# Kernel tuning notes

Measured on AMD Instinct MI355X. Metric: run time of the kernel, lower is better.

## Reference

```python
import jax, jax.numpy as jnp
import numpy as np

NUM_PATCHES = 10
SIGMA = 4.0            # size_exp_deadzone
PAD_X = 16             # padding_deadzone_size_x
PAD_Y = 16             # padding_deadzone_size_y
DEADZONE_EXP = True
HARD_CUTOUT = True     # deadzone_hard_cutout == 1
HARD_CUTOUT_SIZE = 4.0


def setup_inputs() -> dict:
    key = jax.random.key(0)
    k1, k2, k3, k4 = jax.random.split(key, 4)
    B, C, H, W = 8, 1, 256, 256
    D, KH, KW = 64, 1, 33
    inp = {
        "input": jax.random.normal(k1, (B, C, H, W), dtype=jnp.float32),
        "dictionary_filter": jax.random.normal(k2, (64, C, 33, 33), dtype=jnp.float32),
        "dictionary": jax.random.normal(k3, (64, C, 33, 33), dtype=jnp.float32),
        "dictionary_prior": jax.random.uniform(k4, (64,), dtype=jnp.float32),
    }
    return inp


def _fourier_convolution(contour, dictionary_filter):
    # contour: [B,C,H,W], dictionary_filter: [D,C,kh,kw] (kh,kw odd)
    B, C, H, W = contour.shape
    D, _, kh, kw = dictionary_filter.shape
    filt = jnp.flip(dictionary_filter, axis=(-2, -1))
    padded = jnp.zeros((D, C, H, W), dtype=contour.dtype).at[:, :, :kh, :kw].set(filt)
    padded = jnp.roll(padded, shift=(-(kh // 2), -(kw // 2)), axis=(-2, -1))
    filt_fft = jnp.fft.rfft2(padded)                 # [D,C,H,W//2+1]
    contour_fft = jnp.fft.rfft2(contour)             # [B,C,H,W//2+1]
    # [B,D,C,H,W] -> sum over channel C -> [B,D,H,W]
    conv = jnp.fft.irfft2(contour_fft[:, None] * filt_fft[None], s=(H, W)).sum(axis=2)
    return conv


def reference(input, dictionary_filter, dictionary, dictionary_prior):
    B, C, H, W = input.shape
    dt = input.dtype
    conv = _fourier_convolution(input, dictionary_filter)  # [B,D,H,W]

    use_map = jnp.ones((B, H, W), dtype=dt)
    if PAD_X > 0:
        use_map = use_map.at[:, :PAD_X, :].set(0.0).at[:, -PAD_X:, :].set(0.0)
    if PAD_Y > 0:
        use_map = use_map.at[:, :, :PAD_Y].set(0.0).at[:, :, -PAD_Y:].set(0.0)

    xs = jnp.arange(H, dtype=dt)
    ys = jnp.arange(W, dtype=dt)
    batch_idx = jnp.arange(B)

    def step(use_map, _):
        # search tensor: conv * use_map * prior  -> [B,D,H,W]
        search = conv * use_map[:, None] * dictionary_prior[None, :, None, None]
        flat = search.reshape(B, -1)
        idx = jnp.argmax(flat, axis=1)                    # [B]
        ov0 = jnp.max(flat, axis=1)                       # saliency incl. prior
        d = idx // (H * W)
        rem = idx % (H * W)
        px = rem // W
        py = rem % W
        ov1 = conv[batch_idx, d, px, py]                  # raw overlap
        # deadzone centered at (px,py)
        dx = xs[None, :] - px[:, None].astype(dt)         # [B,H]
        dy = ys[None, :] - py[:, None].astype(dt)         # [B,W]
        dist2 = dx[:, :, None] ** 2 + dy[:, None, :] ** 2  # [B,H,W]
        if DEADZONE_EXP:
            tmap = 1.0 - jnp.exp(-dist2 / (2.0 * SIGMA ** 2))
        else:
            tmap = jnp.ones_like(dist2)
        if HARD_CUTOUT:
            tmap = tmap * jnp.where(dist2 <= HARD_CUTOUT_SIZE ** 2, 0.0, 1.0)
        new_use = use_map * tmap
        new_use = new_use / jnp.max(new_use, axis=(1, 2), keepdims=True)
        pos = jnp.stack([d, px, py], axis=1)              # [B,3]
        ov = jnp.stack([ov0, ov1], axis=1)                # [B,2]
        return new_use, (pos, ov)

    _, (pos, ov) = jax.lax.scan(step, use_map, None, length=NUM_PATCHES)
    position_found = jnp.transpose(pos, (1, 0, 2))  # [B, num_patches, 3] int
    overlap_found = jnp.transpose(ov, (1, 0, 2))    # [B, num_patches, 2]
    return position_found, overlap_found
```

## Files before the change

kernel.cpp:

```cpp
#include <hip/hip_runtime.h>

typedef unsigned long long u64;
typedef unsigned int u32;
typedef unsigned short ushort_t;

using f32x16 = __attribute__((ext_vector_type(16))) float;
using f32x4  = __attribute__((ext_vector_type(4))) float;
using short8 = __attribute__((ext_vector_type(8))) short;

#define NB 8
#define NPIX 65536
#define CAND_CAP 65536
#define MARGIN 45.0f

__device__ __forceinline__ u32 fsort(float f){
  u32 u = __float_as_uint(f);
  return (u & 0x80000000u) ? ~u : (u | 0x80000000u);
}
__device__ __forceinline__ float funsort(u32 s){
  u32 u = (s & 0x80000000u) ? (s ^ 0x80000000u) : ~s;
  return __uint_as_float(u);
}
__device__ __forceinline__ u32 rneb(float f){
  u32 x = __float_as_uint(f);
  return (x + 0x7fffu + ((x >> 16) & 1u)) >> 16;
}
__device__ __forceinline__ float bf2f(u32 h){ return __uint_as_float(h << 16); }

__global__ __launch_bounds__(256) void prep_kernel(
    const float* __restrict__ filt, const float* __restrict__ prior,
    ushort_t* __restrict__ afh, ushort_t* __restrict__ acolh,
    float* __restrict__ fcorner, float* __restrict__ priorR,
    float* __restrict__ filtT4, float* __restrict__ filtC,
    u32* __restrict__ ncand, u32* __restrict__ mmax)
{
  int t = blockIdx.x * 256 + threadIdx.x;
  if (t == 0) *ncand = 0u;
  if (t < 8) mmax[t] = 0u;
  for (int i = t; i < 67584; i += 16384){
    int j = i & 7; int fidx = i >> 3; int lane = fidx & 63; int rest = fidx >> 6;
    int dt = rest & 1; int kc = (rest >> 1) & 1; int fy = rest >> 2;
    int d = dt * 32 + (lane & 31);
    int fx = 16 * kc + 8 * (lane >> 5) + j;
    afh[i] = (ushort_t)rneb(filt[d * 1089 + fy * 33 + fx]);
  }
  for (int i = t; i < 2048; i += 16384){
    int j = i & 7; int fidx = i >> 3; int lane = fidx & 63; int rest = fidx >> 6;
    int dt = rest & 1; int kc = rest >> 1;
    int d = dt * 32 + (lane & 31);
    int fy = 16 * kc + 8 * (lane >> 5) + j;
    acolh[i] = (ushort_t)rneb(filt[d * 1089 + fy * 33 + 32]);
  }
  for (int i = t; i < 2048; i += 16384){
    int reg = i & 15; int rest = i >> 4; int lane = rest & 63; int dt = rest >> 6;
    int d = dt * 32 + (reg & 3) + 8 * (reg >> 2) + 4 * (lane >> 5);
    fcorner[i] = filt[d * 1089 + 1088];
    priorR[i] = prior[d];
  }
  for (int i = t; i < 67584; i += 16384){
    int e = i & 3; int d = (i >> 2) & 63; int q = (i >> 8) & 7; int fy = i >> 11;
    filtT4[i] = filt[d * 1089 + fy * 33 + 4 * q + e];
  }
  for (int i = t; i < 2112; i += 16384){
    int d = i & 63; int fy = i >> 6;
    filtC[i] = filt[d * 1089 + fy * 33 + 32];
  }
}

__device__ __forceinline__ u32 funnel(u32 hi, u32 lo, int sh){
  return (u32)((((u64)hi << 32) | (u64)lo) >> sh);
}
template<int J>
__device__ __forceinline__ short8 extractf(uint4 P0, uint4 P1, int sh){
  u32 W[8] = {P0.x, P0.y, P0.z, P0.w, P1.x, P1.y, P1.z, P1.w};
  uint4 t;
  t.x = funnel(W[J + 1], W[J + 0], sh);
  t.y = funnel(W[J + 2], W[J + 1], sh);
  t.z = funnel(W[J + 3], W[J + 2], sh);
  t.w = funnel(W[J + 4], W[J + 3], sh);
  return __builtin_bit_cast(short8, t);
}
__device__ __forceinline__ f32x16 zero16(){
  f32x16 v;
  #pragma unroll
  for (int i = 0; i < 16; ++i) v[i] = 0.f;
  return v;
}

template<int J>
__device__ __forceinline__ void conv_body(
    const char* ldsc, const ushort_t* lds16, int w, int l, int tX,
    const short8* __restrict__ afh8, const short8* __restrict__ acol8,
    const f32x4* __restrict__ fcp, const f32x4* __restrict__ prp,
    u64* __restrict__ pb, int sh)
{
  const int c = l & 31, h = l >> 5;
  const int y0 = w;
  int cob0[2], cob1[2];
  #pragma unroll
  for (int kc = 0; kc < 2; ++kc){
    int yp = (y0 + 8 * c + 16 * kc + 8 * h - 16) & 255;
    int b0 = yp >> 3, b1 = (b0 + 1) & 31;
    cob0[kc] = b0 * 16; cob1[kc] = b1 * 16;
  }
  const int cc = (y0 + 8 * c + 16) & 255;

#define LA(DST, FY)                                                           \
  { _Pragma("unroll")                                                         \
    for (int kc = 0; kc < 2; ++kc)                                            \
      _Pragma("unroll")                                                       \
      for (int dt = 0; dt < 2; ++dt)                                          \
        DST[kc][dt] = afh8[(((FY) * 2 + kc) * 2 + dt) * 64 + l]; }

#define LW(S, ROWI)                                                           \
  { const char* rb_ = ldsc + (ROWI) * 512;                                    \
    s##S##k0p0 = *(const uint4*)(rb_ + cob0[0]);                              \
    s##S##k0p1 = *(const uint4*)(rb_ + cob1[0]);                              \
    s##S##k1p0 = *(const uint4*)(rb_ + cob0[1]);                              \
    s##S##k1p1 = *(const uint4*)(rb_ + cob1[1]); }

#define CPH(SA, SB, ACUR, ANXT, FYP, DOPF)                                    \
  { if (DOPF){ LA(ANXT, FYP) }                                                \
    short8 b0k0 = extractf<J>(s##SA##k0p0, s##SA##k0p1, sh);                  \
    short8 b0k1 = extractf<J>(s##SA##k1p0, s##SA##k1p1, sh);                  \
    short8 b1k0 = extractf<J>(s##SB##k0p0, s##SB##k0p1, sh);                  \
    short8 b1k1 = extractf<J>(s##SB##k1p0, s##SB##k1p1, sh);                  \
    acc[0][0] = __builtin_amdgcn_mfma_f32_32x32x16_bf16(ACUR[0][0], b0k0, acc[0][0], 0, 0, 0); \
    acc[0][0] = __builtin_amdgcn_mfma_f32_32x32x16_bf16(ACUR[1][0], b0k1, acc[0][0], 0, 0, 0); \
    acc[0][1] = __builtin_amdgcn_mfma_f32_32x32x16_bf16(ACUR[0][1], b0k0, acc[0][1], 0, 0, 0); \
    acc[0][1] = __builtin_amdgcn_mfma_f32_32x32x16_bf16(ACUR[1][1], b0k1, acc[0][1], 0, 0, 0); \
    acc[1][0] = __builtin_amdgcn_mfma_f32_32x32x16_bf16(ACUR[0][0], b1k0, acc[1][0], 0, 0, 0); \
    acc[1][0] = __builtin_amdgcn_mfma_f32_32x32x16_bf16(ACUR[1][0], b1k1, acc[1][0], 0, 0, 0); \
    acc[1][1] = __builtin_amdgcn_mfma_f32_32x32x16_bf16(ACUR[0][1], b1k0, acc[1][1], 0, 0, 0); \
    acc[1][1] = __builtin_amdgcn_mfma_f32_32x32x16_bf16(ACUR[1][1], b1k1, acc[1][1], 0, 0, 0); }

  for (int g0 = 0; g0 < 2; ++g0){
    const int r0 = g0 * 2;
    f32x16 acc[2][2];
    #pragma unroll
    for (int nr = 0; nr < 2; ++nr)
      #pragma unroll
      for (int dt = 0; dt < 2; ++dt) acc[nr][dt] = zero16();

    uint4 s0k0p0, s0k0p1, s0k1p0, s0k1p1;
    uint4 s1k0p0, s1k0p1, s1k1p0, s1k1p1;
    short8 aA[2][2], aB[2][2];

    LW(0, r0)
    LW(1, r0 + 1)
    LA(aA, 0)

    #pragma unroll 1
    for (int fy2 = 0; fy2 < 32; fy2 += 2){
      CPH(0, 1, aA, aB, fy2 + 1, true)
      LW(0, r0 + fy2 + 2)
      CPH(1, 0, aB, aA, fy2 + 2, true)
      LW(1, r0 + fy2 + 3)
    }
    CPH(0, 1, aA, aB, 0, false)

    #pragma unroll
    for (int nr = 0; nr < 2; ++nr){
      #pragma unroll
      for (int kc = 0; kc < 2; ++kc){
        int base = (r0 + nr + 16 * kc + 8 * h) * 512 + cc * 2;
        u32 v0 = *(const ushort_t*)(ldsc + base + 0 * 512);
        u32 v1 = *(const ushort_t*)(ldsc + base + 1 * 512);
        u32 v2 = *(const ushort_t*)(ldsc + base + 2 * 512);
        u32 v3 = *(const ushort_t*)(ldsc + base + 3 * 512);
        u32 v4 = *(const ushort_t*)(ldsc + base + 4 * 512);
        u32 v5 = *(const ushort_t*)(ldsc + base + 5 * 512);
        u32 v6 = *(const ushort_t*)(ldsc + base + 6 * 512);
        u32 v7 = *(const ushort_t*)(ldsc + base + 7 * 512);
        uint4 t;
        t.x = v0 | (v1 << 16); t.y = v2 | (v3 << 16);
        t.z = v4 | (v5 << 16); t.w = v6 | (v7 << 16);
        short8 Bc = __builtin_bit_cast(short8, t);
        #pragma unroll
        for (int dt = 0; dt < 2; ++dt)
          acc[nr][dt] = __builtin_amdgcn_mfma_f32_32x32x16_bf16(
              acol8[(kc * 2 + dt) * 64 + l], Bc, acc[nr][dt], 0, 0, 0);
      }
    }

    #pragma unroll
    for (int nr = 0; nr < 2; ++nr){
      float cv = bf2f((u32)lds16[(r0 + nr + 32) * 256 + cc]);
      float bv = -3e38f; int bd = 0;
      #pragma unroll
      for (int dt = 0; dt < 2; ++dt){
        #pragma unroll
        for (int q = 0; q < 4; ++q){
          f32x4 fc4 = fcp[(dt * 64 + l) * 4 + q];
          f32x4 pr4 = prp[(dt * 64 + l) * 4 + q];
          #pragma unroll
          for (int e = 0; e < 4; ++e){
            int reg = q * 4 + e;
            float s = (acc[nr][dt][reg] + fc4[e] * cv) * pr4[e];
            int d = dt * 32 + e + 8 * q + 4 * h;
            if (s > bv || (s == bv && d < bd)){ bv = s; bd = d; }
          }
        }
      }
      int x = tX + r0 + nr;
      int y = y0 + 8 * c;
      u64 key = ((u64)fsort(bv) << 32) | (u64)(63 - bd);
      u64 other = __shfl_xor(key, 32);
      if (other > key) key = other;
      if (h == 0) pb[(x << 8) | y] = key;
    }
  }
#undef CPH
#undef LW
#undef LA
}

__global__ __launch_bounds__(512) void conv_mfma(
    const float* __restrict__ input,
    const ushort_t* __restrict__ afh, const ushort_t* __restrict__ acolh,
    const float* __restrict__ fcorner, const float* __restrict__ priorR,
    u64* __restrict__ packed)
{
  __shared__ ushort_t lds[9216];
  const int bS = blockIdx.x;
  const int b  = blockIdx.y;
  const int tX = bS * 4;
  const int tid = threadIdx.x;

  const float* inb = input + b * NPIX;
  for (int k = tid; k < 1152; k += 512){
    int r = k >> 5, u = k & 31;
    int gx = (tX - 16 + r) & 255;
    const float* src = inb + (gx << 8) + (u << 3);
    float4 v1 = *(const float4*)(src);
    float4 v2 = *(const float4*)(src + 4);
    uint4 t;
    t.x = rneb(v1.x) | (rneb(v1.y) << 16);
    t.y = rneb(v1.z) | (rneb(v1.w) << 16);
    t.z = rneb(v2.x) | (rneb(v2.y) << 16);
    t.w = rneb(v2.z) | (rneb(v2.w) << 16);
    *(uint4*)((char*)lds + r * 512 + u * 16) = t;
  }
  __syncthreads();

  const int w = tid >> 6, l = tid & 63;
  u64* pb = packed + b * NPIX;
  const int sh = 16 * (w & 1);
  const char* ldsc = (const char*)lds;
  const short8* afh8 = (const short8*)afh;
  const short8* acol8 = (const short8*)acolh;
  const f32x4* fcp = (const f32x4*)fcorner;
  const f32x4* prp = (const f32x4*)priorR;

  switch ((w >> 1) & 3){
    case 0: conv_body<0>(ldsc, lds, w, l, tX, afh8, acol8, fcp, prp, pb, sh); break;
    case 1: conv_body<1>(ldsc, lds, w, l, tX, afh8, acol8, fcp, prp, pb, sh); break;
    case 2: conv_body<2>(ldsc, lds, w, l, tX, afh8, acol8, fcp, prp, pb, sh); break;
    default: conv_body<3>(ldsc, lds, w, l, tX, afh8, acol8, fcp, prp, pb, sh); break;
  }
}

__global__ __launch_bounds__(256) void bmax_kernel(const u64* __restrict__ packed,
                                                   u32* __restrict__ mmax){
  const int b = blockIdx.y, blk = blockIdx.x, tid = threadIdx.x;
  const u32* ph = (const u32*)(packed + b * NPIX);
  u32 m = 0;
  for (int k = tid; k < 2048; k += 256) m = max(m, ph[2 * (blk * 2048 + k) + 1]);
  __shared__ u32 red[256];
  red[tid] = m; __syncthreads();
  for (int s = 128; s > 0; s >>= 1){
    if (tid < s) red[tid] = max(red[tid], red[tid + s]);
    __syncthreads();
  }
  if (tid == 0) atomicMax(&mmax[b], red[0]);
}

__global__ __launch_bounds__(256) void collect_kernel(const u64* __restrict__ packed,
    const u32* __restrict__ mmax, u32* __restrict__ ncand, u32* __restrict__ cand){
  const int b = blockIdx.y, blk = blockIdx.x, tid = threadIdx.x;
  float M = funsort(mmax[b]);
  u32 tu = fsort(M - MARGIN);
  const u32* ph = (const u32*)(packed + b * NPIX);
  for (int k = tid; k < 2048; k += 256){
    int p = blk * 2048 + k;
    u32 v = ph[2 * p + 1];
    if (v >= tu){
      u32 slot = atomicAdd(ncand, 1u);
      if (slot < CAND_CAP) cand[slot] = ((u32)b << 16) | (u32)p;
    }
  }
}

__global__ __launch_bounds__(256) void rerank_kernel(
    const float* __restrict__ input, const float* __restrict__ filtT4,
    const float* __restrict__ filtC, const float* __restrict__ prior,
    const u32* __restrict__ ncand, const u32* __restrict__ cand,
    u64* __restrict__ packed)
{
  const int lane = threadIdx.x & 63;
  const int wv = threadIdx.x >> 6;
  int n = (int)min(*ncand, (u32)CAND_CAP);
  float pv = prior[lane];
  for (int i = blockIdx.x * 4 + wv; i < n; i += 4096){
    u32 v = cand[i];
    int b = v >> 16, p = v & 0xffff;
    int px = p >> 8, py = p & 255;
    if (px < 16 || px >= 240 || py < 16 || py >= 240) continue;
    int yc = py - 16;
    float s0 = 0.f, s1 = 0.f, s2 = 0.f, s3 = 0.f;
    for (int fy = 0; fy < 33; ++fy){
      const float* ir = input + b * NPIX + ((px + fy - 16) << 8) + yc;
      const float* ft = filtT4 + fy * 2048 + lane * 4;
      #pragma unroll
      for (int q = 0; q < 8; ++q){
        const float4 fv = *(const float4*)(ft + q * 256);
        s0 = fmaf(fv.x, ir[4*q+0], s0);
        s1 = fmaf(fv.y, ir[4*q+1], s1);
        s2 = fmaf(fv.z, ir[4*q+2], s2);
        s3 = fmaf(fv.w, ir[4*q+3], s3);
      }
      s0 = fmaf(filtC[fy * 64 + lane], ir[32], s0);
    }
    float s = (s0 + s2) + (s1 + s3);
    u64 key = ((u64)fsort(s * pv) << 32) | (u64)(63 - lane);
    #pragma unroll
    for (int off = 32; off; off >>= 1){
      u64 o = __shfl_down(key, off);
      if (o > key) key = o;
    }
    if (lane == 0) packed[b * NPIX + p] = key;
  }
}

__global__ __launch_bounds__(1024) void greedy_kernel(
    const u64* __restrict__ packed, const float* __restrict__ prior,
    float* __restrict__ out)
{
  const int b = blockIdx.x;
  const int tid = threadIdx.x;
  const u64* pb = packed + b * NPIX;
  const u32* ph = (const u32*)pb;

  const int x = tid >> 2;
  const int ybase = (tid & 3) << 6;
  const int pbase = (x << 8) + ybase;

  float s[64];
  const bool rowin = (x >= 16 && x < 240);
  #pragma unroll
  for (int i = 0; i < 64; ++i){
    int y = ybase + i;
    float bvv = funsort(ph[2 * (pbase + i) + 1]);
    s[i] = (rowin && y >= 16 && y < 240) ? bvv : 0.0f;
  }
  float tm = -3e38f; int tp = pbase;
  #pragma unroll
  for (int i = 0; i < 64; ++i){
    if (s[i] > tm){ tm = s[i]; tp = pbase + i; }
  }

  __shared__ u64 warr[16];
  __shared__ int spx, spy;
  if (tid == 0){ spx = -100000; spy = -100000; }
  __syncthreads();

  for (int t = 0; t < 10; ++t){
    const int px = spx, py = spy;
    if (px >= 0){
      int dxr = x - px;
      if (dxr >= -24 && dxr <= 24){
        int lo = py - 24 - ybase;
        int hi = py + 24 - ybase;
        if (lo < 64 && hi >= 0){
          float dx2 = (float)(dxr * dxr);
          tm = -3e38f; tp = pbase;
          #pragma unroll
          for (int i = 0; i < 64; ++i){
            if (i >= lo && i <= hi){
              float dy = (float)(ybase + i - py);
              float d2 = dx2 + dy * dy;
              float tmap = 1.f - __expf(d2 * -0.03125f);
              if (d2 <= 16.f) tmap = 0.f;
              s[i] *= tmap;
            }
            if (s[i] > tm){ tm = s[i]; tp = pbase + i; }
          }
        }
      }
    }
    u64 key = ((u64)fsort(tm) << 32) | (u64)(0xFFFFu ^ (u32)tp);
    #pragma unroll
    for (int off = 32; off; off >>= 1){
      u64 o = __shfl_down(key, off);
      if (o > key) key = o;
    }
    if ((tid & 63) == 0) warr[tid >> 6] = key;
    __syncthreads();
    if (tid < 64){
      u64 k2 = (tid < 16) ? warr[tid] : 0ull;
      #pragma unroll
      for (int off = 8; off; off >>= 1){
        u64 o = __shfl_down(k2, off);
        if (o > k2) k2 = o;
      }
      if (tid == 0){
        int id = 0xFFFF ^ (int)(k2 & 0xFFFFull);
        float v = funsort((u32)(k2 >> 32));
        u64 pk = pb[id];
        int d = 63 - (int)(pk & 63ull);
        float bvv = funsort((u32)(pk >> 32));
        int xx = id >> 8, yy = id & 255;
        out[b * 30 + t * 3 + 0] = (float)d;
        out[b * 30 + t * 3 + 1] = (float)xx;
        out[b * 30 + t * 3 + 2] = (float)yy;
        out[240 + b * 20 + t * 2 + 0] = v;
        out[240 + b * 20 + t * 2 + 1] = bvv / prior[d];
        spx = xx; spy = yy;
      }
    }
    __syncthreads();
  }
}

extern "C" void kernel_launch(void* const* d_in, const int* in_sizes, int n_in,
                              void* d_out, int out_size, void* d_ws, size_t ws_size,
                              hipStream_t stream)
{
  const float* input = (const float*)d_in[0];
  const float* filt  = (const float*)d_in[1];
  const float* prior = (const float*)d_in[3];
  float* out = (float*)d_out;

  char* ws = (char*)d_ws;
  u64*      packed  = (u64*)(ws);
  u32*      ncand   = (u32*)  (ws + 4194304);
  u32*      mmax    = (u32*)  (ws + 4194368);
  ushort_t* afh     = (ushort_t*)(ws + 4194432);
  ushort_t* acolh   = (ushort_t*)(ws + 4329600);
  float*    fcorner = (float*)(ws + 4333696);
  float*    priorR  = (float*)(ws + 4341888);
  u32*      cand    = (u32*)  (ws + 4350080);
  float*    filtT4  = (float*)(ws + 4612224);
  float*    filtC   = (float*)(ws + 4882560);

  prep_kernel<<<64, 256, 0, stream>>>(filt, prior, afh, acolh, fcorner, priorR,
                                      filtT4, filtC, ncand, mmax);
  conv_mfma<<<dim3(64, NB), 512, 0, stream>>>(input, afh, acolh, fcorner, priorR, packed);
  bmax_kernel<<<dim3(32, NB), 256, 0, stream>>>(packed, mmax);
  collect_kernel<<<dim3(32, NB), 256, 0, stream>>>(packed, mmax, ncand, cand);
  rerank_kernel<<<1024, 256, 0, stream>>>(input, filtT4, filtC, prior, ncand, cand, packed);
  greedy_kernel<<<NB, 1024, 0, stream>>>(packed, prior, out);
}
```

Before: 215.8 us.

## Add filter transpose kernel, filter out-of-border candidates early, vectorize greedy loads

Adds a shared-memory transpose kernel so that building filtT4 and filtC in prep reads coalesced data instead of strided filter elements. The candidate collector now drops border pixels before the atomic append, which shrinks the rerank work list. The rerank margin is tightened slightly, and the greedy kernel loads two packed entries per 16-byte read. The extra kernel launch adds overhead, and the smaller margin slightly raises the risk of missing the true argmax.

```diff
diff --git a/kernel.cpp b/kernel.cpp
--- a/kernel.cpp
+++ b/kernel.cpp
@@ -11,7 +11,7 @@
 #define NB 8
 #define NPIX 65536
 #define CAND_CAP 65536
-#define MARGIN 45.0f
+#define MARGIN 44.0f
 
 __device__ __forceinline__ u32 fsort(float f){
   u32 u = __float_as_uint(f);
@@ -27,16 +27,32 @@
 }
 __device__ __forceinline__ float bf2f(u32 h){ return __uint_as_float(h << 16); }
 
+__global__ __launch_bounds__(256) void transpose_kernel(
+    const float* __restrict__ filt, float* __restrict__ filtT,
+    u32* __restrict__ ncand, u32* __restrict__ mmax)
+{
+  __shared__ float T[64][65];
+  const int b = blockIdx.x;
+  const int e0 = b * 64;
+  const int ecnt = min(64, 1089 - e0);
+  const int w = threadIdx.x >> 6, l = threadIdx.x & 63;
+  if (b == 0 && threadIdx.x == 0) *ncand = 0u;
+  if (b == 0 && threadIdx.x < 8) mmax[threadIdx.x] = 0u;
+  for (int d = w; d < 64; d += 4)
+    if (l < ecnt) T[d][l] = filt[d * 1089 + e0 + l];
+  __syncthreads();
+  for (int r = w; r < ecnt; r += 4)
+    filtT[(e0 + r) * 64 + l] = T[l][r];
+}
+
 __global__ __launch_bounds__(256) void prep_kernel(
-    const float* __restrict__ filt, const float* __restrict__ prior,
+    const float* __restrict__ filt, const float* __restrict__ filtT,
+    const float* __restrict__ prior,
     ushort_t* __restrict__ afh, ushort_t* __restrict__ acolh,
     float* __restrict__ fcorner, float* __restrict__ priorR,
-    float* __restrict__ filtT4, float* __restrict__ filtC,
-    u32* __restrict__ ncand, u32* __restrict__ mmax)
+    float* __restrict__ filtT4, float* __restrict__ filtC)
 {
   int t = blockIdx.x * 256 + threadIdx.x;
-  if (t == 0) *ncand = 0u;
-  if (t < 8) mmax[t] = 0u;
   for (int i = t; i < 67584; i += 16384){
     int j = i & 7; int fidx = i >> 3; int lane = fidx & 63; int rest = fidx >> 6;
     int dt = rest & 1; int kc = (rest >> 1) & 1; int fy = rest >> 2;
@@ -59,11 +75,11 @@
   }
   for (int i = t; i < 67584; i += 16384){
     int e = i & 3; int d = (i >> 2) & 63; int q = (i >> 8) & 7; int fy = i >> 11;
-    filtT4[i] = filt[d * 1089 + fy * 33 + 4 * q + e];
+    filtT4[i] = filtT[(fy * 33 + 4 * q + e) * 64 + d];
   }
   for (int i = t; i < 2112; i += 16384){
     int d = i & 63; int fy = i >> 6;
-    filtC[i] = filt[d * 1089 + fy * 33 + 32];
+    filtC[i] = filtT[(fy * 33 + 32) * 64 + d];
   }
 }
 
@@ -278,13 +294,13 @@
 __global__ __launch_bounds__(256) void collect_kernel(const u64* __restrict__ packed,
     const u32* __restrict__ mmax, u32* __restrict__ ncand, u32* __restrict__ cand){
   const int b = blockIdx.y, blk = blockIdx.x, tid = threadIdx.x;
-  float M = funsort(mmax[b]);
-  u32 tu = fsort(M - MARGIN);
+  u32 tu = fsort(funsort(mmax[b]) - MARGIN);
   const u32* ph = (const u32*)(packed + b * NPIX);
   for (int k = tid; k < 2048; k += 256){
     int p = blk * 2048 + k;
+    int px = p >> 8, py = p & 255;
     u32 v = ph[2 * p + 1];
-    if (v >= tu){
+    if (v >= tu && px >= 16 && px < 240 && py >= 16 && py < 240){
       u32 slot = atomicAdd(ncand, 1u);
       if (slot < CAND_CAP) cand[slot] = ((u32)b << 16) | (u32)p;
     }
@@ -304,9 +320,8 @@
   for (int i = blockIdx.x * 4 + wv; i < n; i += 4096){
     u32 v = cand[i];
     int b = v >> 16, p = v & 0xffff;
-    int px = p >> 8, py = p & 255;
-    if (px < 16 || px >= 240 || py < 16 || py >= 240) continue;
-    int yc = py - 16;
+    int px = p >> 8;
+    int yc = (p & 255) - 16;
     float s0 = 0.f, s1 = 0.f, s2 = 0.f, s3 = 0.f;
     for (int fy = 0; fy < 33; ++fy){
       const float* ir = input + b * NPIX + ((px + fy - 16) << 8) + yc;
@@ -339,7 +354,6 @@
   const int b = blockIdx.x;
   const int tid = threadIdx.x;
   const u64* pb = packed + b * NPIX;
-  const u32* ph = (const u32*)pb;
 
   const int x = tid >> 2;
   const int ybase = (tid & 3) << 6;
@@ -348,10 +362,11 @@
   float s[64];
   const bool rowin = (x >= 16 && x < 240);
   #pragma unroll
-  for (int i = 0; i < 64; ++i){
-    int y = ybase + i;
-    float bvv = funsort(ph[2 * (pbase + i) + 1]);
-    s[i] = (rowin && y >= 16 && y < 240) ? bvv : 0.0f;
+  for (int i2 = 0; i2 < 32; ++i2){
+    uint4 two = *(const uint4*)(pb + pbase + 2 * i2);
+    int y = ybase + 2 * i2;
+    s[2*i2+0] = (rowin && y+0 >= 16 && y+0 < 240) ? funsort(two.y) : 0.0f;
+    s[2*i2+1] = (rowin && y+1 >= 16 && y+1 < 240) ? funsort(two.w) : 0.0f;
   }
   float tm = -3e38f; int tp = pbase;
   #pragma unroll
@@ -442,9 +457,11 @@
   u32*      cand    = (u32*)  (ws + 4350080);
   float*    filtT4  = (float*)(ws + 4612224);
   float*    filtC   = (float*)(ws + 4882560);
-
-  prep_kernel<<<64, 256, 0, stream>>>(filt, prior, afh, acolh, fcorner, priorR,
-                                      filtT4, filtC, ncand, mmax);
+  float*    filtT   = (float*)(ws + 4891008);
+
+  transpose_kernel<<<18, 256, 0, stream>>>(filt, filtT, ncand, mmax);
+  prep_kernel<<<64, 256, 0, stream>>>(filt, filtT, prior, afh, acolh,
+                                      fcorner, priorR, filtT4, filtC);
   conv_mfma<<<dim3(64, NB), 512, 0, stream>>>(input, afh, acolh, fcorner, priorR, packed);
   bmax_kernel<<<dim3(32, NB), 256, 0, stream>>>(packed, mmax);
   collect_kernel<<<dim3(32, NB), 256, 0, stream>>>(packed, mmax, ncand, cand);
```

Result: faster. 208.4 us (median of 2 runs) (-3.4%).
